# Kernel optimization log

Measured on AMD Instinct MI355X. Metric: run time of the kernel, lower is better.

## Reference

```python
import jax, jax.numpy as jnp
import numpy as np

DIM = 512
CODEBOOK_SIZE = 8192


def setup_inputs() -> dict:
    key = jax.random.key(0)
    k1, k2 = jax.random.split(key)
    x = jax.random.normal(k1, (8, 1024, DIM), dtype=jnp.float32)
    embed_weight = jax.random.normal(k2, (CODEBOOK_SIZE, DIM), dtype=jnp.float32)
    return {"x": x, "embed_weight": embed_weight}


def reference(x, embed_weight):
    # flatten: [..., d] -> [N, d]
    shape = x.shape
    flatten = x.reshape(-1, shape[-1])                      # [N, d]
    x_sq = jnp.sum(flatten * flatten, axis=1, keepdims=True)        # [N, 1]
    e_sq = jnp.sum(embed_weight * embed_weight, axis=1)[None, :]    # [1, K]
    dist = -(x_sq - 2.0 * jnp.einsum('nd,kd->nk', flatten, embed_weight) + e_sq)
    embed_ind = jnp.argmax(dist, axis=-1)                   # [N]
    embed_ind = embed_ind.reshape(shape[:-1])               # [...,]
    quantize = embed_weight[embed_ind]                      # [..., d]
    return quantize, embed_ind
```

## Files before the change

### kernel.cpp

```cpp
#include <hip/hip_runtime.h>
#include <math.h>

#define DIM      512
#define KC       8192
#define NR       8192
#define BM       128
#define BN       256
#define NT       4
#define CHUNK    (BN*NT)
#define NXB      (KC/CHUNK)
#define KT       (DIM/32)
#define EPS      0.125f
#define MAXW     16384

typedef __attribute__((ext_vector_type(8))) _Float16 f16x8;
typedef __attribute__((ext_vector_type(4))) float f32x4;

#define AS1 __attribute__((address_space(1)))
#define AS3 __attribute__((address_space(3)))

static __device__ __forceinline__ unsigned fkey(float f) {
    unsigned b = __float_as_uint(f);
    return (b & 0x80000000u) ? ~b : (b | 0x80000000u);
}

__global__ void pack_kernel(const float* __restrict__ X, const float* __restrict__ E,
                            _Float16* __restrict__ Xp, _Float16* __restrict__ Ep,
                            float* __restrict__ e_sq, int* __restrict__ fcount) {
    if (blockIdx.x == 0 && blockIdx.y == 0 && threadIdx.x == 0) *fcount = 0;
    const int isE = blockIdx.y;
    const float* src = isE ? E : X;
    _Float16* dst = isE ? Ep : Xp;
    const int t  = threadIdx.x;
    const int rl = t >> 4;
    const int kt = t & 15;
    const int row = blockIdx.x * 16 + rl;

    float4 v[8];
    const float4* p = reinterpret_cast<const float4*>(src + (size_t)row * DIM + kt * 32);
    #pragma unroll
    for (int q = 0; q < 8; ++q) v[q] = p[q];

    _Float16* d = dst + ((size_t)blockIdx.x * 16 + kt) * 512;
    #pragma unroll
    for (int kg = 0; kg < 4; ++kg) {
        const float* vv = reinterpret_cast<const float*>(&v[kg * 2]);
        f16x8 o;
        #pragma unroll
        for (int j = 0; j < 8; ++j) o[j] = (_Float16)vv[j];
        *reinterpret_cast<f16x8*>(d + (rl + 16 * kg) * 8) = o;
    }

    if (isE) {
        const float* vv = reinterpret_cast<const float*>(v);
        float s = 0.f;
        #pragma unroll
        for (int j = 0; j < 32; ++j) s = fmaf(vv[j], vv[j], s);
        #pragma unroll
        for (int mask = 1; mask < 16; mask <<= 1) s += __shfl_xor(s, mask, 64);
        if (kt == 0) e_sq[row] = s;
    }
}

__global__ __launch_bounds__(256, 2)
void vq_mfma_kernel(const _Float16* __restrict__ Xp, const _Float16* __restrict__ Ep,
                    const float* __restrict__ e_sq,
                    float* __restrict__ pbest, float* __restrict__ psec,
                    int* __restrict__ pidx)
{
    __shared__ _Float16 lds[24576];

    const int tid  = threadIdx.x;
    const int lane = tid & 63;
    const int w    = tid >> 6;
    const int wr   = w >> 1;
    const int wc   = w & 1;

    const int bid = blockIdx.x;
    const int cx  = bid & 7;
    const int ry  = bid >> 3;
    const int row0  = ry * BM;
    const int cbase = cx * CHUNK;
    const int rtb  = row0 >> 4;
    const int ctb0 = cbase >> 4;

    float s1[16], s2[16];
    int   i1[16];
    #pragma unroll
    for (int i = 0; i < 16; ++i) { s1[i] = -INFINITY; s2[i] = -INFINITY; i1[i] = 0; }

    for (int nt = 0; nt < NT; ++nt) {
        const int code0 = cbase + nt * BN;
        const int ctb = ctb0 + nt * 16;

        f32x4 acc[4][8];
        #pragma unroll
        for (int m = 0; m < 4; ++m)
            #pragma unroll
            for (int n = 0; n < 8; ++n)
                acc[m][n] = (f32x4){0.f, 0.f, 0.f, 0.f};

        for (int ks = 0; ks < 8; ++ks) {
            const int kt2 = ks * 2;
            #pragma unroll
            for (int i = 0; i < 4; ++i) {
                const int t = w * 4 + i;
                const int rt = t >> 1, ktl = t & 1;
                const _Float16* gp = Xp + (((size_t)(rtb + rt) * KT + kt2 + ktl) << 9) + lane * 8;
                __builtin_amdgcn_global_load_lds(
                    (const AS1 void*)gp, (AS3 void*)(lds + t * 512), 16, 0, 0);
            }
            #pragma unroll
            for (int j = 0; j < 8; ++j) {
                const int b = w * 8 + j;
                const int rt = b >> 1, ktl = b & 1;
                const _Float16* gp = Ep + (((size_t)(ctb + rt) * KT + kt2 + ktl) << 9) + lane * 8;
                __builtin_amdgcn_global_load_lds(
                    (const AS1 void*)gp, (AS3 void*)(lds + 8192 + b * 512), 16, 0, 0);
            }
            __syncthreads();

            #pragma unroll
            for (int kk = 0; kk < 2; ++kk) {
                f16x8 bfrag[8];
                #pragma unroll
                for (int n = 0; n < 8; ++n)
                    bfrag[n] = *reinterpret_cast<const f16x8*>(
                        lds + 8192 + ((wc * 8 + n) * 2 + kk) * 512 + lane * 8);
                #pragma unroll
                for (int m = 0; m < 4; ++m) {
                    const f16x8 afrag = *reinterpret_cast<const f16x8*>(
                        lds + ((wr * 4 + m) * 2 + kk) * 512 + lane * 8);
                    #pragma unroll
                    for (int n = 0; n < 8; ++n)
                        acc[m][n] = __builtin_amdgcn_mfma_f32_16x16x32_f16(
                            afrag, bfrag[n], acc[m][n], 0, 0, 0);
                }
            }
            __syncthreads();
        }

        #pragma unroll
        for (int n = 0; n < 8; ++n) {
            const int code = code0 + wc * 128 + n * 16 + (lane & 15);
            const float esv = e_sq[code];
            #pragma unroll
            for (int m = 0; m < 4; ++m) {
                #pragma unroll
                for (int r = 0; r < 4; ++r) {
                    const float sc = fmaf(2.0f, acc[m][n][r], -esv);
                    const int slot = m * 4 + r;
                    if (sc > s1[slot]) { s2[slot] = s1[slot]; s1[slot] = sc; i1[slot] = code; }
                    else if (sc > s2[slot]) { s2[slot] = sc; }
                    else if (sc == s1[slot]) { s2[slot] = sc; }
                }
            }
        }
    }

    #pragma unroll
    for (int slot = 0; slot < 16; ++slot) {
        #pragma unroll
        for (int mask = 1; mask < 16; mask <<= 1) {
            float t1 = __shfl_xor(s1[slot], mask, 64);
            float t2 = __shfl_xor(s2[slot], mask, 64);
            int   j1 = __shfl_xor(i1[slot], mask, 64);
            if (t1 > s1[slot]) { s2[slot] = fmaxf(s1[slot], t2); s1[slot] = t1; i1[slot] = j1; }
            else if (t1 == s1[slot]) { s2[slot] = fmaxf(s2[slot], fmaxf(t1, t2)); i1[slot] = min(i1[slot], j1); }
            else { s2[slot] = fmaxf(s2[slot], t1); }
        }
    }

    __syncthreads();
    float* reds1 = reinterpret_cast<float*>(&lds[0]);
    float* reds2 = reds1 + BM * 2;
    int*   redi  = reinterpret_cast<int*>(reds2 + BM * 2);

    if ((lane & 15) == 0) {
        #pragma unroll
        for (int m = 0; m < 4; ++m)
            #pragma unroll
            for (int r = 0; r < 4; ++r) {
                const int row = wr * 64 + m * 16 + (lane >> 4) * 4 + r;
                reds1[row * 2 + wc] = s1[m * 4 + r];
                reds2[row * 2 + wc] = s2[m * 4 + r];
                redi [row * 2 + wc] = i1[m * 4 + r];
            }
    }
    __syncthreads();

    if (tid < BM) {
        float a1 = reds1[tid * 2 + 0], a2 = reds2[tid * 2 + 0]; int ai = redi[tid * 2 + 0];
        const float b1 = reds1[tid * 2 + 1], b2 = reds2[tid * 2 + 1]; const int bi = redi[tid * 2 + 1];
        if (b1 > a1)       { a2 = fmaxf(a1, b2); a1 = b1; ai = bi; }
        else if (b1 == a1) { a2 = fmaxf(a2, fmaxf(b1, b2)); ai = min(ai, bi); }
        else               { a2 = fmaxf(a2, b1); }
        const int row = row0 + tid;
        pbest[(size_t)row * NXB + cx] = a1;
        psec [(size_t)row * NXB + cx] = a2;
        pidx [(size_t)row * NXB + cx] = ai;
    }
}

__global__ void reduce_kernel(const float* __restrict__ pbest, const float* __restrict__ psec,
                              const int* __restrict__ pidx,
                              int* __restrict__ final_idx, int* __restrict__ flags,
                              int* __restrict__ fcount, int* __restrict__ wlist,
                              unsigned long long* __restrict__ rkey)
{
    const int row = blockIdx.x * 256 + threadIdx.x;
    float pb[NXB];
    float s1 = -INFINITY, s2 = -INFINITY; int i1 = 0;
    #pragma unroll
    for (int j = 0; j < NXB; ++j) {
        const float t1 = pbest[(size_t)row * NXB + j];
        const float t2 = psec [(size_t)row * NXB + j];
        const int   j1 = pidx [(size_t)row * NXB + j];
        pb[j] = t1;
        if (t1 > s1)       { s2 = fmaxf(s1, t2); s1 = t1; i1 = j1; }
        else if (t1 == s1) { s2 = fmaxf(s2, fmaxf(t1, t2)); i1 = min(i1, j1); }
        else               { s2 = fmaxf(s2, t1); }
    }
    final_idx[row] = i1;
    int fl = 0;
    if (s1 - s2 < EPS) {
        fl = 1;
        rkey[row] = 0ULL;
        #pragma unroll
        for (int j = 0; j < NXB; ++j) {
            if (pb[j] >= s1 - EPS) {
                const int p = atomicAdd(fcount, 1);
                if (p < MAXW) wlist[p] = (row << 4) | j;
            }
        }
    }
    flags[row] = fl;
}

__global__ __launch_bounds__(256)
void rescue_kernel(const float* __restrict__ X, const float* __restrict__ E,
                   const float* __restrict__ e_sq,
                   const int* __restrict__ fcount, const int* __restrict__ wlist,
                   unsigned long long* __restrict__ rkey)
{
    const int nw0 = *fcount;
    const int nw  = nw0 < MAXW ? nw0 : MAXW;
    const int lane = threadIdx.x & 63;
    const int w    = threadIdx.x >> 6;
    const int q    = blockIdx.y;

    for (int e = blockIdx.x; e < nw; e += gridDim.x) {
        const unsigned ent = (unsigned)wlist[e];
        const int row = ent >> 4;
        const int j   = ent & 15;
        if (row >= NR || j >= NXB) continue;

        const float4* xp = reinterpret_cast<const float4*>(X + (size_t)row * DIM) + lane * 2;
        const float4 x0 = xp[0], x1 = xp[1];

        const int c0 = j * CHUNK + q * 256 + w * 64;
        float best = -INFINITY; int bi = 0;
        for (int c = c0; c < c0 + 64; ++c) {
            const float4* ep = reinterpret_cast<const float4*>(E + (size_t)c * DIM) + lane * 2;
            const float4 e0 = ep[0], e1 = ep[1];
            float dot = x0.x * e0.x;
            dot = fmaf(x0.y, e0.y, dot);
            dot = fmaf(x0.z, e0.z, dot);
            dot = fmaf(x0.w, e0.w, dot);
            dot = fmaf(x1.x, e1.x, dot);
            dot = fmaf(x1.y, e1.y, dot);
            dot = fmaf(x1.z, e1.z, dot);
            dot = fmaf(x1.w, e1.w, dot);
            #pragma unroll
            for (int mask = 1; mask < 64; mask <<= 1) dot += __shfl_xor(dot, mask, 64);
            const float s = fmaf(2.f, dot, -e_sq[c]);
            if (s > best) { best = s; bi = c; }
        }
        if (lane == 0) {
            const unsigned long long pk =
                ((unsigned long long)fkey(best) << 32) | (unsigned)(8191 - bi);
            atomicMax(&rkey[row], pk);
        }
    }
}

__global__ void gather_kernel(const int* __restrict__ final_idx,
                              const int* __restrict__ flags,
                              const unsigned long long* __restrict__ rkey,
                              const float* __restrict__ E,
                              float* __restrict__ out_q, float* __restrict__ out_i)
{
    const int row = blockIdx.x;
    __shared__ int s_bi;
    if (threadIdx.x == 0) {
        int bi;
        if (flags[row]) {
            const unsigned long long pk = rkey[row];
            bi = 8191 - (int)(pk & 0xFFFFFFFFull);
        } else {
            bi = final_idx[row];
        }
        s_bi = bi;
        out_i[row] = (float)bi;
    }
    __syncthreads();
    const int bi = s_bi;
    const float4* src = reinterpret_cast<const float4*>(E + (size_t)bi * DIM);
    float4* dst = reinterpret_cast<float4*>(out_q + (size_t)row * DIM);
    dst[threadIdx.x] = src[threadIdx.x];
}

extern "C" void kernel_launch(void* const* d_in, const int* in_sizes, int n_in,
                              void* d_out, int out_size, void* d_ws, size_t ws_size,
                              hipStream_t stream) {
    const float* X = (const float*)d_in[0];
    const float* E = (const float*)d_in[1];

    float* out_q = (float*)d_out;
    float* out_i = (float*)d_out + (size_t)NR * DIM;

    _Float16* Xp = (_Float16*)d_out;
    _Float16* Ep = Xp + (size_t)NR * DIM;

    unsigned long long* rkey = (unsigned long long*)d_ws;
    float* e_sq      = (float*)(rkey + NR);
    float* pbest     = e_sq + KC;
    float* psec      = pbest + (size_t)NR * NXB;
    int*   pidx      = (int*)(psec + (size_t)NR * NXB);
    int*   final_idx = pidx + (size_t)NR * NXB;
    int*   flags     = final_idx + NR;
    int*   wlist     = flags + NR;
    int*   fcount    = wlist + MAXW;

    hipLaunchKernelGGL(pack_kernel, dim3(NR / 16, 2), dim3(256), 0, stream,
                       X, E, Xp, Ep, e_sq, fcount);

    hipLaunchKernelGGL(vq_mfma_kernel, dim3(NXB * (NR / BM)), dim3(256), 0, stream,
                       Xp, Ep, e_sq, pbest, psec, pidx);

    hipLaunchKernelGGL(reduce_kernel, dim3(NR / 256), dim3(256), 0, stream,
                       pbest, psec, pidx, final_idx, flags, fcount, wlist, rkey);

    hipLaunchKernelGGL(rescue_kernel, dim3(1024, 4), dim3(256), 0, stream,
                       X, E, e_sq, fcount, wlist, rkey);

    hipLaunchKernelGGL(gather_kernel, dim3(NR), dim3(128), 0, stream,
                       final_idx, flags, rkey, E, out_q, out_i);
}
```

Baseline: 182.3 us.

## Fuse partial reduction with gather and fix up only ambiguous rows

Replaces the thread-per-row reduce kernel and the separate full gather with one wave-per-row kernel. It merges the 8 partial candidates through lane shuffles and immediately copies the winning codebook row for confident rows. Ambiguous rows go into a compacted list, and a small fixup kernel writes their outputs after the rescue pass. This removes a full-size kernel pass and the flags array, at the cost of an extra atomic counter and a wider reduce grid.

```diff
diff --git a/kernel.cpp b/kernel.cpp
--- a/kernel.cpp
+++ b/kernel.cpp
@@ -26,8 +26,9 @@
 
 __global__ void pack_kernel(const float* __restrict__ X, const float* __restrict__ E,
                             _Float16* __restrict__ Xp, _Float16* __restrict__ Ep,
-                            float* __restrict__ e_sq, int* __restrict__ fcount) {
-    if (blockIdx.x == 0 && blockIdx.y == 0 && threadIdx.x == 0) *fcount = 0;
+                            float* __restrict__ e_sq, int* __restrict__ fcount,
+                            int* __restrict__ fcount2) {
+    if (blockIdx.x == 0 && blockIdx.y == 0 && threadIdx.x == 0) { *fcount = 0; *fcount2 = 0; }
     const int isE = blockIdx.y;
     const float* src = isE ? E : X;
     _Float16* dst = isE ? Ep : Xp;
@@ -202,39 +203,59 @@
     }
 }
 
-__global__ void reduce_kernel(const float* __restrict__ pbest, const float* __restrict__ psec,
-                              const int* __restrict__ pidx,
-                              int* __restrict__ final_idx, int* __restrict__ flags,
-                              int* __restrict__ fcount, int* __restrict__ wlist,
-                              unsigned long long* __restrict__ rkey)
+__global__ __launch_bounds__(256)
+void reduce_gather_kernel(const float* __restrict__ pbest, const float* __restrict__ psec,
+                          const int* __restrict__ pidx, const float* __restrict__ E,
+                          int* __restrict__ final_idx,
+                          int* __restrict__ fcount, int* __restrict__ wlist,
+                          int* __restrict__ fcount2, int* __restrict__ frow2,
+                          unsigned long long* __restrict__ rkey,
+                          float* __restrict__ out_q, float* __restrict__ out_i)
 {
-    const int row = blockIdx.x * 256 + threadIdx.x;
-    float pb[NXB];
-    float s1 = -INFINITY, s2 = -INFINITY; int i1 = 0;
-    #pragma unroll
-    for (int j = 0; j < NXB; ++j) {
-        const float t1 = pbest[(size_t)row * NXB + j];
-        const float t2 = psec [(size_t)row * NXB + j];
-        const int   j1 = pidx [(size_t)row * NXB + j];
-        pb[j] = t1;
-        if (t1 > s1)       { s2 = fmaxf(s1, t2); s1 = t1; i1 = j1; }
-        else if (t1 == s1) { s2 = fmaxf(s2, fmaxf(t1, t2)); i1 = min(i1, j1); }
-        else               { s2 = fmaxf(s2, t1); }
-    }
-    final_idx[row] = i1;
-    int fl = 0;
-    if (s1 - s2 < EPS) {
-        fl = 1;
-        rkey[row] = 0ULL;
-        #pragma unroll
-        for (int j = 0; j < NXB; ++j) {
-            if (pb[j] >= s1 - EPS) {
-                const int p = atomicAdd(fcount, 1);
-                if (p < MAXW) wlist[p] = (row << 4) | j;
-            }
-        }
-    }
-    flags[row] = fl;
+    const int wv   = threadIdx.x >> 6;
+    const int lane = threadIdx.x & 63;
+    const int row  = blockIdx.x * 4 + wv;
+
+    float t1 = -INFINITY, t2 = -INFINITY, own = -INFINITY;
+    int   j1 = 0;
+    if (lane < 8) {
+        t1  = pbest[(size_t)row * NXB + lane];
+        t2  = psec [(size_t)row * NXB + lane];
+        j1  = pidx [(size_t)row * NXB + lane];
+        own = t1;
+    }
+    #pragma unroll
+    for (int mask = 1; mask < 8; mask <<= 1) {
+        const float o1 = __shfl_xor(t1, mask, 64);
+        const float o2 = __shfl_xor(t2, mask, 64);
+        const int   oj = __shfl_xor(j1, mask, 64);
+        if (o1 > t1)       { t2 = fmaxf(t1, o2); t1 = o1; j1 = oj; }
+        else if (o1 == t1) { t2 = fmaxf(t2, fmaxf(o1, o2)); j1 = min(j1, oj); }
+        else               { t2 = fmaxf(t2, o1); }
+    }
+    const int   fl = (t1 - t2 < EPS) ? 1 : 0;
+    const float s1 = __shfl(t1, 0, 64);
+    const int   bi = __shfl(j1, 0, 64);
+    const int   flag = __shfl(fl, 0, 64);
+
+    if (flag) {
+        if (lane < 8 && own >= s1 - EPS) {
+            const int p = atomicAdd(fcount, 1);
+            if (p < MAXW) wlist[p] = (row << 4) | lane;
+        }
+        if (lane == 0) {
+            rkey[row] = 0ULL;
+            final_idx[row] = bi;
+            const int p2 = atomicAdd(fcount2, 1);
+            if (p2 < NR) frow2[p2] = row;
+        }
+    } else {
+        const float4* src = reinterpret_cast<const float4*>(E + (size_t)bi * DIM) + lane * 2;
+        float4* dst = reinterpret_cast<float4*>(out_q + (size_t)row * DIM) + lane * 2;
+        dst[0] = src[0];
+        dst[1] = src[1];
+        if (lane == 0) out_i[row] = (float)bi;
+    }
 }
 
 __global__ __launch_bounds__(256)
@@ -284,30 +305,24 @@
     }
 }
 
-__global__ void gather_kernel(const int* __restrict__ final_idx,
-                              const int* __restrict__ flags,
-                              const unsigned long long* __restrict__ rkey,
-                              const float* __restrict__ E,
-                              float* __restrict__ out_q, float* __restrict__ out_i)
+__global__ __launch_bounds__(128)
+void fixup_kernel(const int* __restrict__ fcount2, const int* __restrict__ frow2,
+                  const unsigned long long* __restrict__ rkey,
+                  const int* __restrict__ final_idx, const float* __restrict__ E,
+                  float* __restrict__ out_q, float* __restrict__ out_i)
 {
-    const int row = blockIdx.x;
-    __shared__ int s_bi;
-    if (threadIdx.x == 0) {
-        int bi;
-        if (flags[row]) {
-            const unsigned long long pk = rkey[row];
-            bi = 8191 - (int)(pk & 0xFFFFFFFFull);
-        } else {
-            bi = final_idx[row];
-        }
-        s_bi = bi;
-        out_i[row] = (float)bi;
-    }
-    __syncthreads();
-    const int bi = s_bi;
-    const float4* src = reinterpret_cast<const float4*>(E + (size_t)bi * DIM);
-    float4* dst = reinterpret_cast<float4*>(out_q + (size_t)row * DIM);
-    dst[threadIdx.x] = src[threadIdx.x];
+    const int nf0 = *fcount2;
+    const int nf  = nf0 < NR ? nf0 : NR;
+    for (int f = blockIdx.x; f < nf; f += gridDim.x) {
+        const int row = frow2[f];
+        if ((unsigned)row >= NR) continue;
+        const unsigned long long pk = rkey[row];
+        int bi = (pk == 0ULL) ? final_idx[row] : (8191 - (int)(pk & 0xFFFFFFFFull));
+        if ((unsigned)bi >= KC) bi = 0;
+        if (threadIdx.x == 0) out_i[row] = (float)bi;
+        const float4* src = reinterpret_cast<const float4*>(E + (size_t)bi * DIM) + threadIdx.x;
+        reinterpret_cast<float4*>(out_q + (size_t)row * DIM)[threadIdx.x] = src[0];
+    }
 }
 
 extern "C" void kernel_launch(void* const* d_in, const int* in_sizes, int n_in,
@@ -328,22 +343,24 @@
     float* psec      = pbest + (size_t)NR * NXB;
     int*   pidx      = (int*)(psec + (size_t)NR * NXB);
     int*   final_idx = pidx + (size_t)NR * NXB;
-    int*   flags     = final_idx + NR;
-    int*   wlist     = flags + NR;
+    int*   frow2     = final_idx + NR;
+    int*   wlist     = frow2 + NR;
     int*   fcount    = wlist + MAXW;
+    int*   fcount2   = fcount + 1;
 
     hipLaunchKernelGGL(pack_kernel, dim3(NR / 16, 2), dim3(256), 0, stream,
-                       X, E, Xp, Ep, e_sq, fcount);
+                       X, E, Xp, Ep, e_sq, fcount, fcount2);
 
     hipLaunchKernelGGL(vq_mfma_kernel, dim3(NXB * (NR / BM)), dim3(256), 0, stream,
                        Xp, Ep, e_sq, pbest, psec, pidx);
 
-    hipLaunchKernelGGL(reduce_kernel, dim3(NR / 256), dim3(256), 0, stream,
-                       pbest, psec, pidx, final_idx, flags, fcount, wlist, rkey);
+    hipLaunchKernelGGL(reduce_gather_kernel, dim3(NR / 4), dim3(256), 0, stream,
+                       pbest, psec, pidx, E, final_idx, fcount, wlist,
+                       fcount2, frow2, rkey, out_q, out_i);
 
     hipLaunchKernelGGL(rescue_kernel, dim3(1024, 4), dim3(256), 0, stream,
                        X, E, e_sq, fcount, wlist, rkey);
 
-    hipLaunchKernelGGL(gather_kernel, dim3(NR), dim3(128), 0, stream,
-                       final_idx, flags, rkey, E, out_q, out_i);
-}
+    hipLaunchKernelGGL(fixup_kernel, dim3(2048), dim3(128), 0, stream,
+                       fcount2, frow2, rkey, final_idx, E, out_q, out_i);
+}
```

New measurement: 179.9 us. About the same (-1.3%).
